# Performance work log

Hardware: AMD Instinct MI355X
Metric: run time of the kernel (lower is better)

Reference implementation:

```python
import jax, jax.numpy as jnp
import numpy as np

N, E = 50000, 640000
FEAT, EMB, HID, B = 128, 128, 512, 32


def setup_inputs() -> dict:
    key = jax.random.key(0)
    ks = jax.random.split(key, 12)
    def w(k, shape, fan_in):
        return jax.random.normal(k, shape, dtype=jnp.float32) / np.sqrt(fan_in)
    return {
        "x": jax.random.normal(ks[0], (N, FEAT), dtype=jnp.float32),
        "edge_index": jax.random.randint(ks[1], (2, E), 0, N, dtype=jnp.int64),
        "last_hidden": jax.random.normal(ks[2], (1, B, HID), dtype=jnp.float32),
        "W1_rel": w(ks[3], (FEAT, EMB), FEAT),
        "W1_root": w(ks[4], (FEAT, EMB), FEAT),
        "b1": jnp.zeros((EMB,), dtype=jnp.float32),
        "W2_rel": w(ks[5], (EMB, EMB), EMB),
        "W2_root": w(ks[6], (EMB, EMB), EMB),
        "b2": jnp.zeros((EMB,), dtype=jnp.float32),
        "Wp": w(ks[7], (HID, EMB), HID),
        "bp": jnp.zeros((EMB,), dtype=jnp.float32),
    }


def _rgcn(h, src, dst, W_rel, W_root, b):
    # transform-then-gather (N < E so cheaper): messages along edges src->dst
    msg = (h @ W_rel)[src]                                   # [E, emb]
    agg = jax.ops.segment_sum(msg, dst, num_segments=N)      # [N, emb]
    deg = jax.ops.segment_sum(jnp.ones((E,), h.dtype), dst, num_segments=N)
    agg = agg / jnp.maximum(deg, 1.0)[:, None]               # mean aggregation (PyG RGCNConv default)
    return agg + h @ W_root + b


def reference(x, edge_index, last_hidden, W1_rel, W1_root, b1, W2_rel, W2_root, b2, Wp, bp):
    src, dst = edge_index[0], edge_index[1]
    h = jax.nn.relu(_rgcn(x, src, dst, W1_rel, W1_root, b1))   # [N, emb]
    h = jax.nn.relu(_rgcn(h, src, dst, W2_rel, W2_root, b2))   # [N, emb]
    message_embed = (last_hidden @ Wp + bp)[0]                 # squeeze(0) -> [B, emb]
    scores = h @ message_embed.T                               # [N, B]
    return jax.nn.log_softmax(scores, axis=0)
```

## Files before the change

kernel.cpp:

```cpp
#include <hip/hip_runtime.h>
#include <hip/hip_bf16.h>

#define N_NODES 50000
#define N_EDGES 640000
#define DUMMY   N_NODES
#define CAP     56
#define NBUCK   196
#define EBLK    2500

typedef __attribute__((ext_vector_type(8))) short short8;
typedef __attribute__((ext_vector_type(4))) float floatx4;

__device__ __forceinline__ float bf2f(unsigned short u) {
    return __uint_as_float(((unsigned int)u) << 16);
}
__device__ __forceinline__ unsigned short f2bf(float x) {
    unsigned int u = __float_as_uint(x);
    u = (u + 0x7fffu + ((u >> 16) & 1u)) >> 16;
    return (unsigned short)u;
}
__device__ __forceinline__ unsigned char f2f8(float x) {
    int pk = __builtin_amdgcn_cvt_pk_fp8_f32(x, x, 0, false);
    return (unsigned char)(pk & 0xff);
}
__device__ __forceinline__ unsigned int pk4_fp8(float x0, float x1, float x2, float x3) {
    int v = __builtin_amdgcn_cvt_pk_fp8_f32(x0, x1, 0, false);
    v = __builtin_amdgcn_cvt_pk_fp8_f32(x2, x3, v, true);
    return (unsigned int)v;
}
__device__ __forceinline__ unsigned int pk2_bf16(float lo, float hi) {
    return (unsigned int)f2bf(lo) | ((unsigned int)f2bf(hi) << 16);
}

__global__ void __launch_bounds__(256) prep_k(const float* __restrict__ W0,
                                              const float* __restrict__ W1,
                                              const float* __restrict__ W2,
                                              const float* __restrict__ W3,
                                              unsigned short* __restrict__ T0,
                                              unsigned short* __restrict__ T1,
                                              unsigned short* __restrict__ T2,
                                              unsigned short* __restrict__ T3,
                                              const float* __restrict__ lh,
                                              const float* __restrict__ Wp,
                                              const float* __restrict__ bp,
                                              unsigned short* __restrict__ meb,
                                              unsigned char* __restrict__ tbf,
                                              const int* __restrict__ dst,
                                              int* __restrict__ blockcnt) {
    __shared__ int h[NBUCK];
    int b = blockIdx.x, tid = threadIdx.x;
    bool is_hist;
    int idx;
    if (b < 546) { is_hist = ((b & 1) == 0); idx = b >> 1; }
    else         { is_hist = true;            idx = 273 + (b - 546); }
    if (is_hist) {
        if (tid < NBUCK) h[tid] = 0;
        __syncthreads();
        int e = idx * 256 + tid;
        int bk = (dst[e] >> 8) & 255;
        if (bk < NBUCK) atomicAdd(&h[bk], 1);
        __syncthreads();
        if (tid < NBUCK) blockcnt[tid * EBLK + idx] = h[tid];
        return;
    }
    int s = idx;
    if (s < 256) {
        int i2 = s * 256 + tid;
        int w = i2 >> 14;
        int r = i2 & 16383;
        int n = r >> 7, k = r & 127;
        const float* W = (w == 0) ? W0 : (w == 1) ? W1 : (w == 2) ? W2 : W3;
        unsigned short* T = (w == 0) ? T0 : (w == 1) ? T1 : (w == 2) ? T2 : T3;
        T[r] = f2bf(W[k * 128 + n]);
    } else if (s < 272) {
        int o = (s - 256) * 256 + tid;
        int i = o >> 7, c = o & 127;
        float acc = bp[c];
        const float4* lr = (const float4*)(lh + i * 512);
        #pragma unroll 4
        for (int k4 = 0; k4 < 128; k4++) {
            float4 v = lr[k4];
            acc += v.x * Wp[(4 * k4 + 0) * 128 + c] + v.y * Wp[(4 * k4 + 1) * 128 + c]
                 + v.z * Wp[(4 * k4 + 2) * 128 + c] + v.w * Wp[(4 * k4 + 3) * 128 + c];
        }
        meb[o] = f2bf(acc);
    } else {
        if (tid < 32) ((unsigned int*)(tbf + (size_t)DUMMY * 128))[tid] = 0;
    }
}

__global__ void __launch_bounds__(256) scan_k(int* __restrict__ blockcnt,
                                              int* __restrict__ totals) {
    __shared__ int sm[256];
    int b = blockIdx.x, t = threadIdx.x;
    int running = 0;
    for (int c = 0; c < 10; c++) {
        int i = c * 256 + t;
        int v = (i < EBLK) ? blockcnt[b * EBLK + i] : 0;
        sm[t] = v;
        __syncthreads();
        for (int off = 1; off < 256; off <<= 1) {
            int u = (t >= off) ? sm[t - off] : 0;
            __syncthreads();
            sm[t] += u;
            __syncthreads();
        }
        if (i < EBLK) blockcnt[b * EBLK + i] = running + sm[t] - v;
        int ctot = sm[255];
        __syncthreads();
        running += ctot;
    }
    if (t == 0) totals[b] = running;
}

__global__ void __launch_bounds__(256) scatter_k(const int* __restrict__ src,
                                                 const int* __restrict__ dst,
                                                 const int* __restrict__ blockcnt,
                                                 const int* __restrict__ totals,
                                                 unsigned int* __restrict__ pairs) {
    __shared__ int offl[NBUCK];
    __shared__ int sm[256];
    int blk = blockIdx.x, t = threadIdx.x;
    int tv = (t < NBUCK) ? totals[t] : 0;
    sm[t] = tv;
    __syncthreads();
    for (int off = 1; off < 256; off <<= 1) {
        int u = (t >= off) ? sm[t - off] : 0;
        __syncthreads();
        sm[t] += u;
        __syncthreads();
    }
    if (t < NBUCK) offl[t] = (sm[t] - tv) + blockcnt[t * EBLK + blk];
    __syncthreads();
    int e = blk * 256 + t;
    int d = dst[e], s = src[e];
    int bk = (d >> 8) & 255;
    if (bk < NBUCK) {
        int pos = atomicAdd(&offl[bk], 1);
        if ((unsigned)pos < (unsigned)N_EDGES)
            pairs[pos] = ((unsigned int)s << 16) | (unsigned int)(d & 0xffff);
    }
}

#define EPI_LD 132
template <bool AF32>
__device__ __forceinline__ void gemm_dual_lds32(int bid, int tid,
                                                const void* __restrict__ Ain,
                                                const unsigned short* __restrict__ BtRel,
                                                const unsigned short* __restrict__ BtRoot,
                                                unsigned char* __restrict__ Trel,
                                                unsigned short* __restrict__ Rootb,
                                                int M, char* __restrict__ pool) {
    int wid = tid >> 6, lane = tid & 63;
    int m = lane & 15, g = lane >> 4;
    int r0 = bid * 32;
    if constexpr (AF32) {
        const float* A = (const float*)Ain;
        #pragma unroll
        for (int j = 0; j < 2; j++) {
            int k = j * 256 + tid;
            int row = k >> 4;
            int grow = r0 + row; grow = (grow < M) ? grow : (M - 1);
            const float* p = A + (size_t)grow * 128 + (k & 15) * 8;
            float4 v0 = *(const float4*)p;
            float4 v1 = *(const float4*)(p + 4);
            short8 t8;
            t8[0] = (short)f2bf(v0.x); t8[1] = (short)f2bf(v0.y);
            t8[2] = (short)f2bf(v0.z); t8[3] = (short)f2bf(v0.w);
            t8[4] = (short)f2bf(v1.x); t8[5] = (short)f2bf(v1.y);
            t8[6] = (short)f2bf(v1.z); t8[7] = (short)f2bf(v1.w);
            *(short8*)(pool + ((k * 16) ^ ((row & 7) << 4))) = t8;
        }
    } else {
        const unsigned short* A = (const unsigned short*)Ain;
        #pragma unroll
        for (int j = 0; j < 2; j++) {
            int k = j * 256 + tid;
            int row = k >> 4;
            int grow = r0 + row; grow = (grow < M) ? grow : (M - 1);
            short8 v = *(const short8*)(A + (size_t)grow * 128 + (k & 15) * 8);
            *(short8*)(pool + ((k * 16) ^ ((row & 7) << 4))) = v;
        }
    }
    #pragma unroll
    for (int j = 0; j < 8; j++) {
        int k = j * 256 + tid;
        int row = k >> 4;
        short8 v = *(const short8*)(BtRel + (size_t)k * 8);
        *(short8*)(pool + 8192 + ((k * 16) ^ ((row & 7) << 4))) = v;
    }
    __syncthreads();
    int lrow = (wid >> 1) * 16 + m;
    int asw = (lrow & 7) << 4, abase = lrow * 256;
    short8 a[4];
    #pragma unroll
    for (int kt = 0; kt < 4; kt++)
        a[kt] = *(const short8*)(pool + ((abase + kt * 64 + g * 16) ^ asw));
    int browbase = (wid & 1) * 64;
    floatx4 accR[4], accO[4];
    #pragma unroll
    for (int ct = 0; ct < 4; ct++) {
        accR[ct] = (floatx4)(0.f);
        int brow = browbase + ct * 16 + m;
        int bbase = brow * 256, bsw = (brow & 7) << 4;
        #pragma unroll
        for (int kt = 0; kt < 4; kt++) {
            short8 bv = *(const short8*)(pool + 8192 + ((bbase + kt * 64 + g * 16) ^ bsw));
            accR[ct] = __builtin_amdgcn_mfma_f32_16x16x32_bf16(a[kt], bv, accR[ct], 0, 0, 0);
        }
    }
    __syncthreads();
    #pragma unroll
    for (int j = 0; j < 8; j++) {
        int k = j * 256 + tid;
        int row = k >> 4;
        short8 v = *(const short8*)(BtRoot + (size_t)k * 8);
        *(short8*)(pool + 8192 + ((k * 16) ^ ((row & 7) << 4))) = v;
    }
    __syncthreads();
    #pragma unroll
    for (int ct = 0; ct < 4; ct++) {
        accO[ct] = (floatx4)(0.f);
        int brow = browbase + ct * 16 + m;
        int bbase = brow * 256, bsw = (brow & 7) << 4;
        #pragma unroll
        for (int kt = 0; kt < 4; kt++) {
            short8 bv = *(const short8*)(pool + 8192 + ((bbase + kt * 64 + g * 16) ^ bsw));
            accO[ct] = __builtin_amdgcn_mfma_f32_16x16x32_bf16(a[kt], bv, accO[ct], 0, 0, 0);
        }
    }
    __syncthreads();
    float* epi = (float*)(pool + 8192);
    int rh = (wid >> 1) * 16, ch = (wid & 1) * 64;
    #pragma unroll
    for (int ct = 0; ct < 4; ct++)
        #pragma unroll
        for (int rg = 0; rg < 4; rg++)
            epi[(rh + g * 4 + rg) * EPI_LD + ch + ct * 16 + m] = accR[ct][rg];
    __syncthreads();
    {
        int lr = tid >> 3, c0 = (tid & 7) * 16;
        int ro = r0 + lr;
        const float* row = epi + lr * EPI_LD + c0;
        if (ro < M) {
            uint4 w;
            w.x = pk4_fp8(row[0],  row[1],  row[2],  row[3]);
            w.y = pk4_fp8(row[4],  row[5],  row[6],  row[7]);
            w.z = pk4_fp8(row[8],  row[9],  row[10], row[11]);
            w.w = pk4_fp8(row[12], row[13], row[14], row[15]);
            *(uint4*)(Trel + (size_t)ro * 128 + c0) = w;
        }
    }
    __syncthreads();
    #pragma unroll
    for (int ct = 0; ct < 4; ct++)
        #pragma unroll
        for (int rg = 0; rg < 4; rg++)
            epi[(rh + g * 4 + rg) * EPI_LD + ch + ct * 16 + m] = accO[ct][rg];
    __syncthreads();
    {
        int lr = tid >> 3, c0 = (tid & 7) * 16;
        int ro = r0 + lr;
        const float* row = epi + lr * EPI_LD + c0;
        if (ro < M) {
            uint4 w0, w1;
            w0.x = pk2_bf16(row[0],  row[1]);
            w0.y = pk2_bf16(row[2],  row[3]);
            w0.z = pk2_bf16(row[4],  row[5]);
            w0.w = pk2_bf16(row[6],  row[7]);
            w1.x = pk2_bf16(row[8],  row[9]);
            w1.y = pk2_bf16(row[10], row[11]);
            w1.z = pk2_bf16(row[12], row[13]);
            w1.w = pk2_bf16(row[14], row[15]);
            *(uint4*)(Rootb + (size_t)ro * 128 + c0) = w0;
            *(uint4*)(Rootb + (size_t)ro * 128 + c0 + 8) = w1;
        }
    }
}

__global__ void __launch_bounds__(256) placegemm_k(const int* __restrict__ totals,
                                                   const unsigned int* __restrict__ pairs,
                                                   unsigned short* __restrict__ ssrc,
                                                   int* __restrict__ cnt,
                                                   const float* __restrict__ A,
                                                   const unsigned short* __restrict__ BtRel,
                                                   const unsigned short* __restrict__ BtRoot,
                                                   unsigned char* __restrict__ Trel,
                                                   unsigned short* __restrict__ Rootb) {
    __shared__ __align__(16) char pool[40960];
    int t = threadIdx.x;
    if (blockIdx.x >= NBUCK) {
        gemm_dual_lds32<true>(blockIdx.x - NBUCK, t, A, BtRel, BtRoot,
                              Trel, Rootb, N_NODES, pool);
        return;
    }
    int b = blockIdx.x;
    int* lcnt = (int*)pool;
    int* sm   = (int*)(pool + 1024);
    int* sb   = (int*)(pool + 2048);
    int tv = (t < NBUCK) ? totals[t] : 0;
    sm[t] = tv;
    __syncthreads();
    for (int off = 1; off < 256; off <<= 1) {
        int u = (t >= off) ? sm[t - off] : 0;
        __syncthreads();
        sm[t] += u;
        __syncthreads();
    }
    if (t == b) *sb = sm[t] - tv;
    lcnt[t] = 0;
    __syncthreads();
    int base = *sb;
    int n = totals[b];
    if (n > N_EDGES) n = N_EDGES;
    for (int i = t; i < n; i += 256) {
        int gi = base + i;
        if ((unsigned)gi >= (unsigned)N_EDGES) break;
        unsigned int p = pairs[gi];
        int dl = (int)(p & 0xffu);
        int d = b * 256 + dl;
        int s = (int)(p >> 16);
        int r = atomicAdd(&lcnt[dl], 1);
        if (d < N_NODES && r < CAP)
            ssrc[(size_t)d * CAP + r] = (unsigned short)s;
    }
    __syncthreads();
    int node = b * 256 + t;
    if (node < N_NODES) cnt[node] = lcnt[t];
}

__global__ void __launch_bounds__(256) gemm_dual_k(const unsigned short* __restrict__ A,
                                                   const unsigned short* __restrict__ BtRel,
                                                   const unsigned short* __restrict__ BtRoot,
                                                   unsigned char* __restrict__ Trel,
                                                   unsigned short* __restrict__ Rootb, int M) {
    __shared__ __align__(16) char pool[40960];
    gemm_dual_lds32<false>(blockIdx.x, threadIdx.x, A, BtRel, BtRoot, Trel, Rootb, M, pool);
}

__global__ void __launch_bounds__(256) agg_k(const int* __restrict__ cnt,
                                             const unsigned short* __restrict__ ssrc,
                                             const unsigned char* __restrict__ t,
                                             const unsigned short* __restrict__ rootb,
                                             const float* __restrict__ bias,
                                             unsigned short* __restrict__ hout) {
    int node = blockIdx.x * 4 + (threadIdx.x >> 6);
    if (node >= N_NODES) return;
    int lane = threadIdx.x & 63;
    int fl = lane & 31;
    int sh = (lane & 32) >> 1;
    int beg = node * CAP;
    int deg = cnt[node];
    deg = (deg < CAP) ? deg : CAP;
    int pad = (deg + 7) & ~7;
    const unsigned char* tf = t + fl * 4;
    float a0=0.f,a1=0.f,a2=0.f,a3=0.f;
    float b0=0.f,b1=0.f,b2=0.f,b3=0.f;
    int s0base = sh >> 4;
    for (int k = 0; k < pad; k += 16) {
        const unsigned short* sp = ssrc + beg + k;
        uint4 w0 = *(const uint4*)sp;
        uint4 w1 = (k + 8 < pad) ? *(const uint4*)(sp + 8) : make_uint4(0u, 0u, 0u, 0u);
        int s0 = k + s0base;
        int i0 = (s0 +  0 < deg) ? (int)((w0.x >> sh) & 0xffffu) : DUMMY;
        int i1 = (s0 +  2 < deg) ? (int)((w0.y >> sh) & 0xffffu) : DUMMY;
        int i2 = (s0 +  4 < deg) ? (int)((w0.z >> sh) & 0xffffu) : DUMMY;
        int i3 = (s0 +  6 < deg) ? (int)((w0.w >> sh) & 0xffffu) : DUMMY;
        int i4 = (s0 +  8 < deg) ? (int)((w1.x >> sh) & 0xffffu) : DUMMY;
        int i5 = (s0 + 10 < deg) ? (int)((w1.y >> sh) & 0xffffu) : DUMMY;
        int i6 = (s0 + 12 < deg) ? (int)((w1.z >> sh) & 0xffffu) : DUMMY;
        int i7 = (s0 + 14 < deg) ? (int)((w1.w >> sh) & 0xffffu) : DUMMY;
        unsigned int u0 = *(const unsigned int*)(tf + (size_t)i0 * 128);
        unsigned int u1 = *(const unsigned int*)(tf + (size_t)i1 * 128);
        unsigned int u2 = *(const unsigned int*)(tf + (size_t)i2 * 128);
        unsigned int u3 = *(const unsigned int*)(tf + (size_t)i3 * 128);
        unsigned int u4 = *(const unsigned int*)(tf + (size_t)i4 * 128);
        unsigned int u5 = *(const unsigned int*)(tf + (size_t)i5 * 128);
        unsigned int u6 = *(const unsigned int*)(tf + (size_t)i6 * 128);
        unsigned int u7 = *(const unsigned int*)(tf + (size_t)i7 * 128);
        a0 += __builtin_amdgcn_cvt_f32_fp8(u0, 0) + __builtin_amdgcn_cvt_f32_fp8(u1, 0);
        a1 += __builtin_amdgcn_cvt_f32_fp8(u0, 1) + __builtin_amdgcn_cvt_f32_fp8(u1, 1);
        a2 += __builtin_amdgcn_cvt_f32_fp8(u0, 2) + __builtin_amdgcn_cvt_f32_fp8(u1, 2);
        a3 += __builtin_amdgcn_cvt_f32_fp8(u0, 3) + __builtin_amdgcn_cvt_f32_fp8(u1, 3);
        b0 += __builtin_amdgcn_cvt_f32_fp8(u2, 0) + __builtin_amdgcn_cvt_f32_fp8(u3, 0);
        b1 += __builtin_amdgcn_cvt_f32_fp8(u2, 1) + __builtin_amdgcn_cvt_f32_fp8(u3, 1);
        b2 += __builtin_amdgcn_cvt_f32_fp8(u2, 2) + __builtin_amdgcn_cvt_f32_fp8(u3, 2);
        b3 += __builtin_amdgcn_cvt_f32_fp8(u2, 3) + __builtin_amdgcn_cvt_f32_fp8(u3, 3);
        a0 += __builtin_amdgcn_cvt_f32_fp8(u4, 0) + __builtin_amdgcn_cvt_f32_fp8(u5, 0);
        a1 += __builtin_amdgcn_cvt_f32_fp8(u4, 1) + __builtin_amdgcn_cvt_f32_fp8(u5, 1);
        a2 += __builtin_amdgcn_cvt_f32_fp8(u4, 2) + __builtin_amdgcn_cvt_f32_fp8(u5, 2);
        a3 += __builtin_amdgcn_cvt_f32_fp8(u4, 3) + __builtin_amdgcn_cvt_f32_fp8(u5, 3);
        b0 += __builtin_amdgcn_cvt_f32_fp8(u6, 0) + __builtin_amdgcn_cvt_f32_fp8(u7, 0);
        b1 += __builtin_amdgcn_cvt_f32_fp8(u6, 1) + __builtin_amdgcn_cvt_f32_fp8(u7, 1);
        b2 += __builtin_amdgcn_cvt_f32_fp8(u6, 2) + __builtin_amdgcn_cvt_f32_fp8(u7, 2);
        b3 += __builtin_amdgcn_cvt_f32_fp8(u6, 3) + __builtin_amdgcn_cvt_f32_fp8(u7, 3);
    }
    a0 += b0; a1 += b1; a2 += b2; a3 += b3;
    a0 += __shfl_xor(a0, 32);
    a1 += __shfl_xor(a1, 32);
    a2 += __shfl_xor(a2, 32);
    a3 += __shfl_xor(a3, 32);
    if ((lane & 32) == 0) {
        float inv = 1.f / fmaxf((float)deg, 1.f);
        int f = fl * 4;
        ushort4 r = *(const ushort4*)(rootb + (size_t)node * 128 + f);
        float4 bb = *(const float4*)(bias + f);
        ushort4 o;
        o.x = f2bf(fmaxf(a0 * inv + bf2f(r.x) + bb.x, 0.f));
        o.y = f2bf(fmaxf(a1 * inv + bf2f(r.y) + bb.y, 0.f));
        o.z = f2bf(fmaxf(a2 * inv + bf2f(r.z) + bb.z, 0.f));
        o.w = f2bf(fmaxf(a3 * inv + bf2f(r.w) + bb.w, 0.f));
        *(ushort4*)(hout + (size_t)node * 128 + f) = o;
    }
}

__global__ void __launch_bounds__(256) scores_cs_k(const unsigned short* __restrict__ A,
                                                   const unsigned short* __restrict__ Bt,
                                                   float* __restrict__ S,
                                                   float* __restrict__ pm,
                                                   float* __restrict__ ps) {
    __shared__ float Sl[64][33];
    __shared__ float sm[256], ss[256];
    int tid = threadIdx.x;
    int wid = tid >> 6, lane = tid & 63;
    int r0 = blockIdx.x * 64 + wid * 16;
    int m = lane & 15, g = lane >> 4;
    int row = r0 + m;
    int rowc = (row < N_NODES) ? row : (N_NODES - 1);
    short8 a[4];
    #pragma unroll
    for (int kt = 0; kt < 4; kt++)
        a[kt] = *(const short8*)(A + (size_t)rowc * 128 + kt * 32 + g * 8);
    floatx4 acc[2];
    acc[0] = (floatx4)(0.f);
    acc[1] = (floatx4)(0.f);
    #pragma unroll
    for (int ct = 0; ct < 2; ct++) {
        const unsigned short* b = Bt + (size_t)(ct * 16 + m) * 128 + g * 8;
        #pragma unroll
        for (int kt = 0; kt < 4; kt++) {
            short8 bv = *(const short8*)(b + kt * 32);
            acc[ct] = __builtin_amdgcn_mfma_f32_16x16x32_bf16(a[kt], bv, acc[ct], 0, 0, 0);
        }
    }
    #pragma unroll
    for (int ct = 0; ct < 2; ct++) {
        #pragma unroll
        for (int rg = 0; rg < 4; rg++) {
            int lr = wid * 16 + g * 4 + rg;
            int ro = r0 + g * 4 + rg;
            Sl[lr][ct * 16 + m] = acc[ct][rg];
            if (ro < N_NODES) S[(size_t)ro * 32 + ct * 16 + m] = acc[ct][rg];
        }
    }
    __syncthreads();
    int col = tid & 31, sub = tid >> 5;
    int blkbase = blockIdx.x * 64;
    float mm = -3.4e38f, s = 0.f;
    for (int r = sub; r < 64; r += 8) {
        if (blkbase + r < N_NODES) {
            float v = Sl[r][col];
            if (v > mm) { s = s * __expf(mm - v) + 1.f; mm = v; }
            else        { s += __expf(v - mm); }
        }
    }
    sm[tid] = mm; ss[tid] = s;
    __syncthreads();
    for (int off = 128; off >= 32; off >>= 1) {
        if (tid < off) {
            float m2 = sm[tid + off], s2 = ss[tid + off];
            float M = fmaxf(sm[tid], m2);
            ss[tid] = ss[tid] * __expf(sm[tid] - M) + s2 * __expf(m2 - M);
            sm[tid] = M;
        }
        __syncthreads();
    }
    if (tid < 32) { pm[tid * 782 + blockIdx.x] = sm[tid]; ps[tid * 782 + blockIdx.x] = ss[tid]; }
}

__global__ void __launch_bounds__(256) merge_k(const float* __restrict__ pm,
                                               const float* __restrict__ ps,
                                               float* __restrict__ cmg,
                                               float* __restrict__ clg) {
    __shared__ float sm[256], ss[256];
    int col = blockIdx.x;
    int t = threadIdx.x;
    float m = -3.4e38f, s = 0.f;
    for (int c = t; c < 782; c += 256) {
        float m2 = pm[col * 782 + c], s2 = ps[col * 782 + c];
        float M = fmaxf(m, m2);
        s = s * __expf(m - M) + s2 * __expf(m2 - M);
        m = M;
    }
    sm[t] = m; ss[t] = s;
    __syncthreads();
    for (int off = 128; off > 0; off >>= 1) {
        if (t < off) {
            float m2 = sm[t + off], s2 = ss[t + off];
            float M = fmaxf(sm[t], m2);
            ss[t] = ss[t] * __expf(sm[t] - M) + s2 * __expf(m2 - M);
            sm[t] = M;
        }
        __syncthreads();
    }
    if (t == 0) { cmg[col] = sm[0]; clg[col] = logf(ss[0]); }
}

__global__ void __launch_bounds__(256) final_k(const float* __restrict__ S,
                                               const float* __restrict__ cmg,
                                               const float* __restrict__ clg,
                                               float* __restrict__ out) {
    __shared__ float cc[32];
    int t = threadIdx.x;
    if (t < 32) cc[t] = cmg[t] + clg[t];
    __syncthreads();
    int idx = blockIdx.x * 256 + t;
    if (idx < N_NODES * 32) {
        int b = idx & 31;
        out[idx] = S[idx] - cc[b];
    }
}

extern "C" void kernel_launch(void* const* d_in, const int* in_sizes, int n_in,
                              void* d_out, int out_size, void* d_ws, size_t ws_size,
                              hipStream_t stream) {
    const float* x       = (const float*)d_in[0];
    const int*   ei      = (const int*)d_in[1];
    const float* lh      = (const float*)d_in[2];
    const float* W1_rel  = (const float*)d_in[3];
    const float* W1_root = (const float*)d_in[4];
    const float* b1      = (const float*)d_in[5];
    const float* W2_rel  = (const float*)d_in[6];
    const float* W2_root = (const float*)d_in[7];
    const float* b2      = (const float*)d_in[8];
    const float* Wp      = (const float*)d_in[9];
    const float* bp      = (const float*)d_in[10];
    float* out = (float*)d_out;
    float* ws  = (float*)d_ws;

    unsigned char*  tbf   = (unsigned char*)(ws + 3200000);
    unsigned short* rootb = (unsigned short*)(ws + 4800032);
    unsigned short* hb    = (unsigned short*)(ws + 8000032);
    unsigned short* Wt1r  = (unsigned short*)(ws + 11200032);
    unsigned short* Wt1o  = (unsigned short*)(ws + 11208224);
    unsigned short* Wt2r  = (unsigned short*)(ws + 11216416);
    unsigned short* Wt2o  = (unsigned short*)(ws + 11224608);
    unsigned short* MEb   = (unsigned short*)(ws + 11232800);
    float* pm   = ws + 11234848;
    float* ps   = ws + 11259872;
    float* cmg  = ws + 11284896;
    float* clg  = ws + 11284928;
    int*   cnt  = (int*)(ws + 11284960);
    int*   blockcnt = (int*)(ws + 11384964);
    int*   totals   = (int*)(ws + 11874964);
    unsigned int* pairs = (unsigned int*)(ws + 11875220);
    float* S    = ws + 12519964;
    unsigned short* ssrc = (unsigned short*)(ws + 12519964);

    const int* srcp = ei;
    const int* dstp = ei + N_EDGES;

    const int ew_grid  = (N_NODES * 32 + 255) / 256;
    const int agg_grid = (N_NODES + 3) / 4;
    const int mm_grid  = (N_NODES + 63) / 64;
    const int g32_grid = (N_NODES + 31) / 32;

    prep_k<<<2773, 256, 0, stream>>>(W1_rel, W1_root, W2_rel, W2_root,
                                     Wt1r, Wt1o, Wt2r, Wt2o,
                                     lh, Wp, bp, MEb, tbf, dstp, blockcnt);

    scan_k<<<NBUCK, 256, 0, stream>>>(blockcnt, totals);

    scatter_k<<<EBLK, 256, 0, stream>>>(srcp, dstp, blockcnt, totals, pairs);

    placegemm_k<<<NBUCK + g32_grid, 256, 0, stream>>>(totals, pairs, ssrc, cnt,
                                                      x, Wt1r, Wt1o, tbf, rootb);

    agg_k<<<agg_grid, 256, 0, stream>>>(cnt, ssrc, tbf, rootb, b1, hb);

    gemm_dual_k<<<g32_grid, 256, 0, stream>>>(hb, Wt2r, Wt2o, tbf, rootb, N_NODES);

    agg_k<<<agg_grid, 256, 0, stream>>>(cnt, ssrc, tbf, rootb, b2, hb);

    scores_cs_k<<<mm_grid, 256, 0, stream>>>(hb, MEb, S, pm, ps);

    merge_k<<<32, 256, 0, stream>>>(pm, ps, cmg, clg);

    final_k<<<ew_grid, 256, 0, stream>>>(S, cmg, clg, out);
}
```

Measured before the change: 219.3 us.

## Fuse second-layer aggregation with score computation and per-block softmax partials

Merges the layer-2 aggregation kernel and the scores/column-softmax kernel into one. Each 4-node block keeps its ReLU'd hidden rows in LDS and computes the 32 scores with scalar FMAs against an LDS copy of the message embedding. This drops the bf16 hidden write and reread plus one launch. In exchange it gives up MFMA for the score GEMM, reloads the embedding into LDS in every one of 12500 blocks, and makes merge_k reduce 12500 partials per column instead of 782. Workspace buffers are rearranged so S and the partials fit.

Result: slower. 230.7 us (+5.2%).

```diff
diff --git a/kernel.cpp b/kernel.cpp
--- a/kernel.cpp
+++ b/kernel.cpp
@@ -7,6 +7,7 @@
 #define CAP     56
 #define NBUCK   196
 #define EBLK    2500
+#define NCHUNK  12500
 
 typedef __attribute__((ext_vector_type(8))) short short8;
 typedef __attribute__((ext_vector_type(4))) float floatx4;
@@ -338,15 +339,12 @@
     gemm_dual_lds32<false>(blockIdx.x, threadIdx.x, A, BtRel, BtRoot, Trel, Rootb, M, pool);
 }
 
-__global__ void __launch_bounds__(256) agg_k(const int* __restrict__ cnt,
-                                             const unsigned short* __restrict__ ssrc,
-                                             const unsigned char* __restrict__ t,
-                                             const unsigned short* __restrict__ rootb,
-                                             const float* __restrict__ bias,
-                                             unsigned short* __restrict__ hout) {
-    int node = blockIdx.x * 4 + (threadIdx.x >> 6);
-    if (node >= N_NODES) return;
-    int lane = threadIdx.x & 63;
+__device__ __forceinline__ void agg_core(int node, int lane,
+                                         const int* __restrict__ cnt,
+                                         const unsigned short* __restrict__ ssrc,
+                                         const unsigned char* __restrict__ t,
+                                         float& A0, float& A1, float& A2, float& A3,
+                                         int& DEG) {
     int fl = lane & 31;
     int sh = (lane & 32) >> 1;
     int beg = node * CAP;
@@ -400,9 +398,23 @@
     a1 += __shfl_xor(a1, 32);
     a2 += __shfl_xor(a2, 32);
     a3 += __shfl_xor(a3, 32);
+    A0 = a0; A1 = a1; A2 = a2; A3 = a3; DEG = deg;
+}
+
+__global__ void __launch_bounds__(256) agg_k(const int* __restrict__ cnt,
+                                             const unsigned short* __restrict__ ssrc,
+                                             const unsigned char* __restrict__ t,
+                                             const unsigned short* __restrict__ rootb,
+                                             const float* __restrict__ bias,
+                                             unsigned short* __restrict__ hout) {
+    int node = blockIdx.x * 4 + (threadIdx.x >> 6);
+    if (node >= N_NODES) return;
+    int lane = threadIdx.x & 63;
+    float a0, a1, a2, a3; int deg;
+    agg_core(node, lane, cnt, ssrc, t, a0, a1, a2, a3, deg);
     if ((lane & 32) == 0) {
         float inv = 1.f / fmaxf((float)deg, 1.f);
-        int f = fl * 4;
+        int f = (lane & 31) * 4;
         ushort4 r = *(const ushort4*)(rootb + (size_t)node * 128 + f);
         float4 bb = *(const float4*)(bias + f);
         ushort4 o;
@@ -414,68 +426,67 @@
     }
 }
 
-__global__ void __launch_bounds__(256) scores_cs_k(const unsigned short* __restrict__ A,
-                                                   const unsigned short* __restrict__ Bt,
+#define MEB_LD 132
+__global__ void __launch_bounds__(256) aggscores_k(const int* __restrict__ cnt,
+                                                   const unsigned short* __restrict__ ssrc,
+                                                   const unsigned char* __restrict__ t,
+                                                   const unsigned short* __restrict__ rootb,
+                                                   const float* __restrict__ bias,
+                                                   const unsigned short* __restrict__ meb,
                                                    float* __restrict__ S,
                                                    float* __restrict__ pm,
                                                    float* __restrict__ ps) {
-    __shared__ float Sl[64][33];
-    __shared__ float sm[256], ss[256];
+    __shared__ unsigned short mebL[32 * MEB_LD];
+    __shared__ float hL[4][128];
+    __shared__ float sL[4][32];
     int tid = threadIdx.x;
-    int wid = tid >> 6, lane = tid & 63;
-    int r0 = blockIdx.x * 64 + wid * 16;
-    int m = lane & 15, g = lane >> 4;
-    int row = r0 + m;
-    int rowc = (row < N_NODES) ? row : (N_NODES - 1);
-    short8 a[4];
-    #pragma unroll
-    for (int kt = 0; kt < 4; kt++)
-        a[kt] = *(const short8*)(A + (size_t)rowc * 128 + kt * 32 + g * 8);
-    floatx4 acc[2];
-    acc[0] = (floatx4)(0.f);
-    acc[1] = (floatx4)(0.f);
-    #pragma unroll
-    for (int ct = 0; ct < 2; ct++) {
-        const unsigned short* b = Bt + (size_t)(ct * 16 + m) * 128 + g * 8;
-        #pragma unroll
-        for (int kt = 0; kt < 4; kt++) {
-            short8 bv = *(const short8*)(b + kt * 32);
-            acc[ct] = __builtin_amdgcn_mfma_f32_16x16x32_bf16(a[kt], bv, acc[ct], 0, 0, 0);
-        }
-    }
-    #pragma unroll
-    for (int ct = 0; ct < 2; ct++) {
-        #pragma unroll
-        for (int rg = 0; rg < 4; rg++) {
-            int lr = wid * 16 + g * 4 + rg;
-            int ro = r0 + g * 4 + rg;
-            Sl[lr][ct * 16 + m] = acc[ct][rg];
-            if (ro < N_NODES) S[(size_t)ro * 32 + ct * 16 + m] = acc[ct][rg];
-        }
-    }
-    __syncthreads();
-    int col = tid & 31, sub = tid >> 5;
-    int blkbase = blockIdx.x * 64;
-    float mm = -3.4e38f, s = 0.f;
-    for (int r = sub; r < 64; r += 8) {
-        if (blkbase + r < N_NODES) {
-            float v = Sl[r][col];
-            if (v > mm) { s = s * __expf(mm - v) + 1.f; mm = v; }
-            else        { s += __expf(v - mm); }
-        }
-    }
-    sm[tid] = mm; ss[tid] = s;
-    __syncthreads();
-    for (int off = 128; off >= 32; off >>= 1) {
-        if (tid < off) {
-            float m2 = sm[tid + off], s2 = ss[tid + off];
-            float M = fmaxf(sm[tid], m2);
-            ss[tid] = ss[tid] * __expf(sm[tid] - M) + s2 * __expf(m2 - M);
-            sm[tid] = M;
-        }
-        __syncthreads();
-    }
-    if (tid < 32) { pm[tid * 782 + blockIdx.x] = sm[tid]; ps[tid * 782 + blockIdx.x] = ss[tid]; }
+    {
+        int row = tid >> 3, c0 = (tid & 7) * 16;
+        const ushort4* gp = (const ushort4*)(meb + row * 128 + c0);
+        ushort4* lp = (ushort4*)(&mebL[row * MEB_LD + c0]);
+        lp[0] = gp[0]; lp[1] = gp[1]; lp[2] = gp[2]; lp[3] = gp[3];
+    }
+    int node = blockIdx.x * 4 + (tid >> 6);
+    int lane = tid & 63;
+    float a0, a1, a2, a3; int deg;
+    agg_core(node, lane, cnt, ssrc, t, a0, a1, a2, a3, deg);
+    if ((lane & 32) == 0) {
+        float inv = 1.f / fmaxf((float)deg, 1.f);
+        int f = (lane & 31) * 4;
+        ushort4 r = *(const ushort4*)(rootb + (size_t)node * 128 + f);
+        float4 bb = *(const float4*)(bias + f);
+        int nl = tid >> 6;
+        hL[nl][f + 0] = bf2f(f2bf(fmaxf(a0 * inv + bf2f(r.x) + bb.x, 0.f)));
+        hL[nl][f + 1] = bf2f(f2bf(fmaxf(a1 * inv + bf2f(r.y) + bb.y, 0.f)));
+        hL[nl][f + 2] = bf2f(f2bf(fmaxf(a2 * inv + bf2f(r.z) + bb.z, 0.f)));
+        hL[nl][f + 3] = bf2f(f2bf(fmaxf(a3 * inv + bf2f(r.w) + bb.w, 0.f)));
+    }
+    __syncthreads();
+    if (tid < 128) {
+        int nl = tid >> 5, b = tid & 31;
+        const float* hp = hL[nl];
+        const unsigned short* mp = &mebL[b * MEB_LD];
+        float acc = 0.f;
+        #pragma unroll 8
+        for (int f = 0; f < 128; f++) acc += hp[f] * bf2f(mp[f]);
+        sL[nl][b] = acc;
+    }
+    __syncthreads();
+    if (tid < 128) {
+        int nl = tid >> 5, b = tid & 31;
+        S[(size_t)(blockIdx.x * 4 + nl) * 32 + b] = sL[nl][b];
+    }
+    if (tid < 32) {
+        float m = sL[0][tid], s = 1.f;
+        #pragma unroll
+        for (int r = 1; r < 4; r++) {
+            float v = sL[r][tid];
+            if (v > m) { s = s * __expf(m - v) + 1.f; m = v; }
+            else       { s += __expf(v - m); }
+        }
+        pm[tid * NCHUNK + blockIdx.x] = m;
+        ps[tid * NCHUNK + blockIdx.x] = s;
+    }
 }
 
 __global__ void __launch_bounds__(256) merge_k(const float* __restrict__ pm,
@@ -486,8 +497,8 @@
     int col = blockIdx.x;
     int t = threadIdx.x;
     float m = -3.4e38f, s = 0.f;
-    for (int c = t; c < 782; c += 256) {
-        float m2 = pm[col * 782 + c], s2 = ps[col * 782 + c];
+    for (int c = t; c < NCHUNK; c += 256) {
+        float m2 = pm[col * NCHUNK + c], s2 = ps[col * NCHUNK + c];
         float M = fmaxf(m, m2);
         s = s * __expf(m - M) + s2 * __expf(m2 - M);
         m = M;
@@ -541,20 +552,20 @@
     unsigned char*  tbf   = (unsigned char*)(ws + 3200000);
     unsigned short* rootb = (unsigned short*)(ws + 4800032);
     unsigned short* hb    = (unsigned short*)(ws + 8000032);
+    float* S = ws + 8000032;
     unsigned short* Wt1r  = (unsigned short*)(ws + 11200032);
     unsigned short* Wt1o  = (unsigned short*)(ws + 11208224);
     unsigned short* Wt2r  = (unsigned short*)(ws + 11216416);
     unsigned short* Wt2o  = (unsigned short*)(ws + 11224608);
     unsigned short* MEb   = (unsigned short*)(ws + 11232800);
-    float* pm   = ws + 11234848;
-    float* ps   = ws + 11259872;
     float* cmg  = ws + 11284896;
     float* clg  = ws + 11284928;
     int*   cnt  = (int*)(ws + 11284960);
     int*   blockcnt = (int*)(ws + 11384964);
     int*   totals   = (int*)(ws + 11874964);
     unsigned int* pairs = (unsigned int*)(ws + 11875220);
-    float* S    = ws + 12519964;
+    float* pm = ws + 11384964;
+    float* ps = ws + 11784964;
     unsigned short* ssrc = (unsigned short*)(ws + 12519964);
 
     const int* srcp = ei;
@@ -562,7 +573,6 @@
 
     const int ew_grid  = (N_NODES * 32 + 255) / 256;
     const int agg_grid = (N_NODES + 3) / 4;
-    const int mm_grid  = (N_NODES + 63) / 64;
     const int g32_grid = (N_NODES + 31) / 32;
 
     prep_k<<<2773, 256, 0, stream>>>(W1_rel, W1_root, W2_rel, W2_root,
@@ -580,9 +590,8 @@
 
     gemm_dual_k<<<g32_grid, 256, 0, stream>>>(hb, Wt2r, Wt2o, tbf, rootb, N_NODES);
 
-    agg_k<<<agg_grid, 256, 0, stream>>>(cnt, ssrc, tbf, rootb, b2, hb);
-
-    scores_cs_k<<<mm_grid, 256, 0, stream>>>(hb, MEb, S, pm, ps);
+    aggscores_k<<<agg_grid, 256, 0, stream>>>(cnt, ssrc, tbf, rootb, b2,
+                                              MEb, S, pm, ps);
 
     merge_k<<<32, 256, 0, stream>>>(pm, ps, cmg, clg);
 
```
